# Optimization experiments

Measured on AMD Instinct MI355X. Metric: run time of the kernel, lower is better.

Reference implementation:

```python
import jax, jax.numpy as jnp
import numpy as np

PAD = 0
B, S = 8, 256
V, E, H = 32000, 512, 1024


def setup_inputs() -> dict:
    key = jax.random.key(0)
    ks = jax.random.split(key, 8)
    s = lambda k, shape, fan: jax.random.normal(k, shape, dtype=jnp.float32) / np.sqrt(fan)
    return {
        "x": jax.random.randint(ks[0], (B, S), 0, V, dtype=jnp.int32),
        "emb_W": s(ks[1], (V, E), E),          # embedding table, shared with generator
        "W_ih": s(ks[2], (3 * H, E), E),        # GRU input->gates (r,z,n)
        "W_hh": s(ks[3], (3 * H, H), H),        # GRU hidden->gates
        "b_ih": jnp.zeros((3 * H,), jnp.float32),
        "b_hh": jnp.zeros((3 * H,), jnp.float32),
        "lin_W": s(ks[4], (E, H + E), H + E),   # linear_logit
        "lin_b": jnp.zeros((E,), jnp.float32),
    }


def _gru(emb, mask, W_ih, W_hh, b_ih, b_hh):
    # emb: [B,S,E], mask: [B,S] True at PAD. Returns ctx [B,S,H].
    gx = jnp.einsum('bse,ge->bsg', emb, W_ih) + b_ih  # [B,S,3H] precomputed input gates
    gx_t = jnp.swapaxes(gx, 0, 1)                      # [S,B,3H]
    m_t = jnp.swapaxes(mask, 0, 1)                     # [S,B]

    def step(h, inp):
        g_x, m = inp
        g_h = h @ W_hh.T + b_hh
        xr, xz, xn = jnp.split(g_x, 3, axis=-1)
        hr, hz, hn = jnp.split(g_h, 3, axis=-1)
        r = jax.nn.sigmoid(xr + hr)
        z = jax.nn.sigmoid(xz + hz)
        n = jnp.tanh(xn + r * hn)
        h_new = (1.0 - z) * n + z * h
        h = jnp.where(m[:, None], h, h_new)            # carry hidden through PAD steps
        out = jnp.where(m[:, None], 0.0, h)            # packed-seq outputs are 0 at PAD
        return h, out

    h0 = jnp.zeros((emb.shape[0], W_hh.shape[1]), emb.dtype)
    _, ctx = jax.lax.scan(step, h0, (gx_t, m_t))
    return jnp.swapaxes(ctx, 0, 1)                     # [B,S,H]


def reference(x, emb_W, W_ih, W_hh, b_ih, b_hh, lin_W, lin_b):
    mask = (x == PAD)
    emb = emb_W[x]                                     # [B,S,E]
    ctx = _gru(emb, mask, W_ih, W_hh, b_ih, b_hh)      # [B,S,H]
    feat = jnp.concatenate([ctx, emb], axis=-1)        # [B,S,H+E]
    logits = jnp.tanh(feat @ lin_W.T + lin_b)          # [B,S,E]
    scores = logits @ emb_W.T                          # [B,S,V] shared-weight generator
    return jax.nn.log_softmax(scores, axis=-1)
```

## Files before the change

### kernel.cpp

```cpp
#include <hip/hip_runtime.h>

typedef unsigned int u32;
typedef unsigned short u16;
typedef unsigned long long u64;
typedef __attribute__((ext_vector_type(8))) short short8;
typedef __attribute__((ext_vector_type(4))) float floatx4;

#define BB 8
#define SS 256
#define VV 32000
#define EE 512
#define HH 1024
#define GRU_BLOCKS 64
#define GRU_THREADS 192
#define NCHUNK 500

__device__ __forceinline__ float b2f(u16 h) {
  union { u32 u; float f; } c; c.u = ((u32)h) << 16; return c.f;
}
__device__ __forceinline__ u16 f2b_bits(u32 u) {
  return (u16)((u + 0x7FFFu + ((u >> 16) & 1u)) >> 16);
}
__device__ __forceinline__ u16 f2b(float f) {
  union { float f; u32 u; } c; c.f = f; return f2b_bits(c.u);
}

__global__ __launch_bounds__(256) void k_detect(const u32* __restrict__ w, int* __restrict__ dflag) {
  __shared__ int cnt;
  if (threadIdx.x == 0) cnt = 0;
  __syncthreads();
  int c = 0;
  for (int i = threadIdx.x; i < 8192; i += 256) {
    u32 e8 = (w[i] >> 7) & 0xFF;
    c += (e8 >= 100 && e8 <= 144);
  }
  atomicAdd(&cnt, c);
  __syncthreads();
  if (threadIdx.x == 0) dflag[0] = (cnt * 2 > 8192) ? 1 : 0;
}

__global__ __launch_bounds__(256) void k_conv(const void* __restrict__ src, u16* __restrict__ dst,
                                              int n, const int* __restrict__ dflag) {
  int i = (blockIdx.x * 256 + threadIdx.x) * 8;
  if (i >= n) return;
  if (dflag[0]) {
    *(uint4*)(dst + i) = *(const uint4*)((const u16*)src + i);
  } else {
    const float* s = (const float*)src + i;
    uint4 a = *(const uint4*)s, b = *(const uint4*)(s + 4);
    u32 w0 = ((u32)f2b_bits(a.y) << 16) | f2b_bits(a.x);
    u32 w1 = ((u32)f2b_bits(a.w) << 16) | f2b_bits(a.z);
    u32 w2 = ((u32)f2b_bits(b.y) << 16) | f2b_bits(b.x);
    u32 w3 = ((u32)f2b_bits(b.w) << 16) | f2b_bits(b.z);
    uint4 r; r.x = w0; r.y = w1; r.z = w2; r.w = w3;
    *(uint4*)(dst + i) = r;
  }
}

__global__ __launch_bounds__(256) void k_init(u32* h_tag, u32* flags, int* dflag, int setflag) {
  int t = threadIdx.x;
  for (int i = t; i < 2 * 8192; i += 256) h_tag[i] = 0;
  if (t < 128) flags[t] = 0;
  if (t == 0 && setflag >= 0) dflag[0] = setflag;
}

__global__ __launch_bounds__(64) void k_gather(const int* __restrict__ x,
                                               const u16* __restrict__ embW,
                                               u16* __restrict__ emb,
                                               u16* __restrict__ feat) {
  int row = blockIdx.x, l = threadIdx.x;
  int tok = x[row];
  uint4 v = ((const uint4*)(embW + (size_t)tok * EE))[l];
  ((uint4*)(emb + (size_t)row * EE))[l] = v;
  ((uint4*)(feat + (size_t)row * 1536 + HH))[l] = v;
}

template <int KTOT>
__device__ __forceinline__ void gemm_core(const u16* __restrict__ A, int lda,
                                          const u16* __restrict__ Bm, int ldb,
                                          int m0, int n0, floatx4 acc[4][4]) {
  __shared__ __align__(16) u16 As[128 * 64];
  __shared__ __align__(16) u16 Bs[128 * 64];
  const int tid = threadIdx.x;
  const int lane = tid & 63, w = tid >> 6;
  const int wm = w & 1, wn = w >> 1;
  const int col16 = lane & 15, quad = lane >> 4;
  floatx4 z = {0.f, 0.f, 0.f, 0.f};
  for (int i = 0; i < 4; i++)
    for (int j = 0; j < 4; j++) acc[i][j] = z;

  for (int k0 = 0; k0 < KTOT; k0 += 64) {
#pragma unroll
    for (int i = 0; i < 4; i++) {
      int c = tid + i * 256;
      int r = c >> 3, off = (c & 7) * 8;
      *(uint4*)&As[r * 64 + off] = *(const uint4*)&A[(size_t)(m0 + r) * lda + k0 + off];
      *(uint4*)&Bs[r * 64 + off] = *(const uint4*)&Bm[(size_t)(n0 + r) * ldb + k0 + off];
    }
    __syncthreads();
#pragma unroll
    for (int kk = 0; kk < 2; kk++) {
      short8 af[4], bf[4];
#pragma unroll
      for (int i = 0; i < 4; i++) {
        af[i] = *(const short8*)&As[(wm * 64 + i * 16 + col16) * 64 + kk * 32 + quad * 8];
        bf[i] = *(const short8*)&Bs[(wn * 64 + i * 16 + col16) * 64 + kk * 32 + quad * 8];
      }
#pragma unroll
      for (int i = 0; i < 4; i++)
#pragma unroll
        for (int j = 0; j < 4; j++)
          acc[i][j] = __builtin_amdgcn_mfma_f32_16x16x32_bf16(af[i], bf[j], acc[i][j], 0, 0, 0);
    }
    __syncthreads();
  }
}

__global__ __launch_bounds__(256) void k_gx(const u16* __restrict__ emb,
                                            const u16* __restrict__ W_ih,
                                            const u16* __restrict__ b_ih,
                                            float* __restrict__ gx2) {
  floatx4 acc[4][4];
  int bm = blockIdx.x, bn = blockIdx.y;
  gemm_core<EE>(emb, EE, W_ih, EE, bm * 128, bn * 128, acc);
  const int tid = threadIdx.x, lane = tid & 63, w = tid >> 6;
  const int wm = w & 1, wn = w >> 1, col16 = lane & 15, quad = lane >> 4;
#pragma unroll
  for (int j = 0; j < 4; j++) {
    int g = bn * 128 + wn * 64 + j * 16 + col16;
    float bias = b2f(b_ih[g]);
    int grp = g >> 10, colh = g & 1023;
    int gb = colh >> 4, slot = grp * 16 + (colh & 15);
#pragma unroll
    for (int i = 0; i < 4; i++)
#pragma unroll
      for (int e = 0; e < 4; e++) {
        int row = bm * 128 + wm * 64 + i * 16 + quad * 4 + e;
        int b = row >> 8, s = row & 255;
        gx2[((size_t)(s * 64 + gb) * 48 + slot) * 8 + b] = acc[i][j][e] + bias;
      }
  }
}

__global__ __launch_bounds__(GRU_THREADS) void k_gru(const u16* __restrict__ W_hh,
                                                     const u16* __restrict__ b_hh,
                                                     const int* __restrict__ x,
                                                     const float* __restrict__ gx2,
                                                     u32* __restrict__ h_tag,
                                                     u32* __restrict__ flags,
                                                     u16* __restrict__ feat) {
  __shared__ __align__(16) u16 h_lds[16][1032];
  __shared__ float gh[3][16][8];
  __shared__ float hold[16][8];
  __shared__ float bhh[48];
  __shared__ int x_s[2048];

  const int tid = threadIdx.x;
  const int lane = tid & 63, w = tid >> 6;
  const int blk = blockIdx.x, hc = blk * 16;
  const int col16 = lane & 15, quad = lane >> 4;

  for (int i = tid; i < 16 * 1032; i += GRU_THREADS) ((u16*)h_lds)[i] = 0;
  for (int i = tid; i < 2048; i += GRU_THREADS) x_s[i] = x[i];
  if (tid < 128) hold[tid & 15][tid >> 4] = 0.f;
  if (tid < 48) bhh[tid] = b2f(b_hh[(tid >> 4) * HH + hc + (tid & 15)]);

  short8 Wf[32];
  {
    int grow = w * HH + hc + col16;
    const u16* wp = W_hh + (size_t)grow * HH + quad * 8;
#pragma unroll
    for (int t = 0; t < 32; t++) Wf[t] = *(const short8*)(wp + t * 32);
  }
  __syncthreads();

  const int cj = tid & 15, cb = tid >> 4;
#pragma unroll 1
  for (int s = 0; s < SS; s++) {
    float xr = 0.f, xz = 0.f, xn = 0.f;
    if (tid < 128) {
      const float* gp = gx2 + (size_t)(s * 64 + blk) * 384;
      xr = gp[cj * 8 + cb];
      xz = gp[128 + cj * 8 + cb];
      xn = gp[256 + cj * 8 + cb];
    }
    if (tid < 64 && tid != blk) {
      const u32* fp = flags + (s & 1) * 64 + tid;
      int guard = 0;
      while (__hip_atomic_load(fp, __ATOMIC_RELAXED, __HIP_MEMORY_SCOPE_AGENT) != (u32)s) {
        if (++guard > (1 << 20)) break;
      }
    }
    __syncthreads();
    {
      const u64* hb = (const u64*)(h_tag + (size_t)(s & 1) * 8192);
      const u32 want = (u32)(s & 0xFFFF);
      u64 vals[22];
      u32 pend = 0;
#pragma unroll
      for (int i = 0; i < 22; i++) {
        int pr = tid + i * GRU_THREADS;
        if (pr < 4096 && ((pr & 511) >> 3) != blk) pend |= 1u << i;
      }
      int guard = 0;
      while (pend) {
#pragma unroll
        for (int i = 0; i < 22; i++)
          if (pend & (1u << i))
            vals[i] = __hip_atomic_load(hb + (tid + i * GRU_THREADS),
                                        __ATOMIC_RELAXED, __HIP_MEMORY_SCOPE_AGENT);
#pragma unroll
        for (int i = 0; i < 22; i++)
          if (pend & (1u << i)) {
            u64 v = vals[i];
            if ((u32)(v & 0xFFFFu) == want && ((u32)(v >> 32) & 0xFFFFu) == want) {
              int pr = tid + i * GRU_THREADS;
              u32 packed = ((u32)(v >> 16) & 0xFFFFu) | ((u32)(v >> 48) << 16);
              *(u32*)&h_lds[pr >> 9][(pr & 511) * 2] = packed;
              pend &= ~(1u << i);
            }
          }
        if (pend) {
          if (++guard > (1 << 14)) break;
        }
      }
    }
    __syncthreads();
    {
      const u16* hp = &h_lds[col16][quad * 8];
      floatx4 a0 = {0.f, 0.f, 0.f, 0.f}, a1 = {0.f, 0.f, 0.f, 0.f};
#pragma unroll
      for (int t = 0; t < 32; t += 2) {
        short8 f0 = *(const short8*)(hp + t * 32);
        short8 f1 = *(const short8*)(hp + t * 32 + 32);
        a0 = __builtin_amdgcn_mfma_f32_16x16x32_bf16(f0, Wf[t], a0, 0, 0, 0);
        a1 = __builtin_amdgcn_mfma_f32_16x16x32_bf16(f1, Wf[t + 1], a1, 0, 0, 0);
      }
      a0 += a1;
      if (quad < 2) {
#pragma unroll
        for (int e = 0; e < 4; e++) gh[w][col16][quad * 4 + e] = a0[e];
      }
    }
    __syncthreads();
    if (tid < 128) {
      float hr = gh[0][cj][cb] + bhh[cj];
      float hz = gh[1][cj][cb] + bhh[16 + cj];
      float hn = gh[2][cj][cb] + bhh[32 + cj];
      float r = 1.f / (1.f + __expf(-(xr + hr)));
      float z = 1.f / (1.f + __expf(-(xz + hz)));
      float tn = xn + r * hn;
      float n = 1.f - 2.f / (1.f + __expf(2.f * tn));
      float ho = hold[cj][cb];
      float hnew = (1.f - z) * n + z * ho;
      int pad = (x_s[cb * SS + s] == 0);
      if (pad) hnew = ho;
      hold[cj][cb] = hnew;
      u16 hb16 = f2b(hnew);
      u32 tw = ((u32)hb16 << 16) | (u32)((s + 1) & 0xFFFF);
      __hip_atomic_store(h_tag + (size_t)((s + 1) & 1) * 8192 + cb * 1024 + hc + cj, tw,
                         __ATOMIC_RELAXED, __HIP_MEMORY_SCOPE_AGENT);
      h_lds[cb][hc + cj] = hb16;
      feat[(size_t)(cb * SS + s) * 1536 + hc + cj] = pad ? (u16)0 : hb16;
    }
    if (tid == 0)
      __hip_atomic_store(flags + ((s + 1) & 1) * 64 + blk, (u32)(s + 1),
                         __ATOMIC_RELAXED, __HIP_MEMORY_SCOPE_AGENT);
  }
}

__global__ __launch_bounds__(256) void k_lin(const u16* __restrict__ feat,
                                             const u16* __restrict__ lin_W,
                                             const u16* __restrict__ lin_b,
                                             u16* __restrict__ logits) {
  floatx4 acc[4][4];
  int bm = blockIdx.x, bn = blockIdx.y;
  gemm_core<1536>(feat, 1536, lin_W, 1536, bm * 128, bn * 128, acc);
  const int tid = threadIdx.x, lane = tid & 63, w = tid >> 6;
  const int wm = w & 1, wn = w >> 1, col16 = lane & 15, quad = lane >> 4;
#pragma unroll
  for (int j = 0; j < 4; j++) {
    int col = bn * 128 + wn * 64 + j * 16 + col16;
    float bias = b2f(lin_b[col]);
#pragma unroll
    for (int i = 0; i < 4; i++)
#pragma unroll
      for (int e = 0; e < 4; e++) {
        int row = bm * 128 + wm * 64 + i * 16 + quad * 4 + e;
        logits[(size_t)row * EE + col] = f2b(tanhf(acc[i][j][e] + bias));
      }
  }
}

__global__ __launch_bounds__(256) void k_scores(const u16* __restrict__ logits,
                                                const u16* __restrict__ embW,
                                                void* __restrict__ outv,
                                                float* __restrict__ partial,
                                                const int* __restrict__ dflag) {
  floatx4 acc[4][4];
  int bm = blockIdx.x, bn = blockIdx.y;
  gemm_core<EE>(logits, EE, embW, EE, bm * 128, bn * 128, acc);
  const int tid = threadIdx.x, lane = tid & 63, w = tid >> 6;
  const int wm = w & 1, wn = w >> 1, col16 = lane & 15, quad = lane >> 4;
  const int bf = dflag[0];
  u16* out16 = (u16*)outv;
  float* out32 = (float*)outv;
#pragma unroll
  for (int i = 0; i < 4; i++) {
#pragma unroll
    for (int e = 0; e < 4; e++) {
      int row = bm * 128 + wm * 64 + i * 16 + quad * 4 + e;
      size_t ob = (size_t)row * VV + bn * 128 + wn * 64;
      float sl = 0.f;
#pragma unroll
      for (int j = 0; j < 4; j++) {
        float v = acc[i][j][e];
        if (bf) out16[ob + j * 16 + col16] = f2b(v);
        else    out32[ob + j * 16 + col16] = v;
        sl += __expf(v);
      }
      sl += __shfl_xor(sl, 1, 64);
      sl += __shfl_xor(sl, 2, 64);
      sl += __shfl_xor(sl, 4, 64);
      sl += __shfl_xor(sl, 8, 64);
      if (col16 == 0) partial[(size_t)row * NCHUNK + bn * 2 + wn] = sl;
    }
  }
}

__global__ __launch_bounds__(64) void k_lse(const float* __restrict__ partial,
                                            float* __restrict__ lse) {
  int row = blockIdx.x, lane = threadIdx.x;
  float s = 0.f;
  for (int c = lane; c < NCHUNK; c += 64) s += partial[(size_t)row * NCHUNK + c];
#pragma unroll
  for (int d = 32; d >= 1; d >>= 1) s += __shfl_xor(s, d, 64);
  if (lane == 0) lse[row] = logf(s);
}

__global__ __launch_bounds__(256) void k_fix(void* __restrict__ outv,
                                             const float* __restrict__ lse,
                                             const int* __restrict__ dflag) {
  int g = blockIdx.x * 256 + threadIdx.x;
  if (dflag[0]) {
    if (g >= 8192000) return;
    u16* out = (u16*)outv;
    int row = g / 4000;
    float l = lse[row];
    uint4 v = ((const uint4*)out)[g];
    u32 a[4] = {v.x, v.y, v.z, v.w};
#pragma unroll
    for (int k = 0; k < 4; k++) {
      float lo = b2f((u16)(a[k] & 0xffff)) - l;
      float hi = b2f((u16)(a[k] >> 16)) - l;
      a[k] = ((u32)f2b(hi) << 16) | (u32)f2b(lo);
    }
    uint4 r; r.x = a[0]; r.y = a[1]; r.z = a[2]; r.w = a[3];
    ((uint4*)out)[g] = r;
  } else {
    float* out = (float*)outv;
    int row = g / 8000;
    float l = lse[row];
    float4 v = ((const float4*)out)[g];
    v.x -= l; v.y -= l; v.z -= l; v.w -= l;
    ((float4*)out)[g] = v;
  }
}

extern "C" void kernel_launch(void* const* d_in, const int* in_sizes, int n_in,
                              void* d_out, int out_size, void* d_ws, size_t ws_size,
                              hipStream_t stream) {
  const int* x = (const int*)d_in[0];

  char* ws = (char*)d_ws;
  float* gx2     = (float*)(ws);
  u16*   feat    = (u16*)(ws + 25165824);
  u16*   emb     = (u16*)(ws + 31457280);
  u16*   logits  = (u16*)(ws + 33554432);
  u32*   h_tag   = (u32*)(ws + 35651584);
  float* partial = (float*)(ws + 35717120);
  float* lse     = (float*)(ws + 39813120);
  u32*   flags   = (u32*)(ws + 39813120);
  int*   dflag   = (int*)(ws + 39821312);
  u16*   embW_c  = (u16*)(ws + 39821568);
  u16*   Wih_c   = (u16*)(ws + 72589568);
  u16*   Whh_c   = (u16*)(ws + 75735296);
  u16*   linW_c  = (u16*)(ws + 82026752);
  u16*   bih_c   = (u16*)(ws + 83599616);
  u16*   bhh_c   = (u16*)(ws + 83605760);
  u16*   linb_c  = (u16*)(ws + 83611904);
  const size_t TOTAL_WS = 83612928;

  const u16 *embW, *W_ih, *W_hh, *b_ih, *b_hh, *lin_W, *lin_b;
  if (ws_size >= TOTAL_WS) {
    k_detect<<<1, 256, 0, stream>>>((const u32*)d_in[1], dflag);
    k_init<<<1, 256, 0, stream>>>(h_tag, flags, dflag, -1);
    k_conv<<<8000, 256, 0, stream>>>(d_in[1], embW_c, VV * EE, dflag);
    k_conv<<<1536, 256, 0, stream>>>(d_in[3], Whh_c, 3 * HH * HH, dflag);
    k_conv<<<768,  256, 0, stream>>>(d_in[2], Wih_c, 3 * HH * EE, dflag);
    k_conv<<<384,  256, 0, stream>>>(d_in[6], linW_c, EE * (HH + EE), dflag);
    k_conv<<<2,    256, 0, stream>>>(d_in[4], bih_c, 3 * HH, dflag);
    k_conv<<<2,    256, 0, stream>>>(d_in[5], bhh_c, 3 * HH, dflag);
    k_conv<<<1,    256, 0, stream>>>(d_in[7], linb_c, EE, dflag);
    embW = embW_c; W_ih = Wih_c; W_hh = Whh_c; b_ih = bih_c;
    b_hh = bhh_c; lin_W = linW_c; lin_b = linb_c;
  } else {
    k_init<<<1, 256, 0, stream>>>(h_tag, flags, dflag, 1);
    embW = (const u16*)d_in[1]; W_ih = (const u16*)d_in[2]; W_hh = (const u16*)d_in[3];
    b_ih = (const u16*)d_in[4]; b_hh = (const u16*)d_in[5];
    lin_W = (const u16*)d_in[6]; lin_b = (const u16*)d_in[7];
  }

  k_gather<<<2048, 64, 0, stream>>>(x, embW, emb, feat);
  k_gx<<<dim3(16, 24), 256, 0, stream>>>(emb, W_ih, b_ih, gx2);
  k_gru<<<GRU_BLOCKS, GRU_THREADS, 0, stream>>>(W_hh, b_hh, x, gx2, h_tag, flags, feat);
  k_lin<<<dim3(16, 4), 256, 0, stream>>>(feat, lin_W, lin_b, logits);
  k_scores<<<dim3(16, 250), 256, 0, stream>>>(logits, embW, d_out, partial, dflag);
  k_lse<<<2048, 64, 0, stream>>>(partial, lse);
  k_fix<<<64000, 256, 0, stream>>>(d_out, lse, dflag);
}
```

Baseline: 1.807 ms.

## Fuse GRU, linear and scores into persistent kernel overlapping chunks

Merges the GRU recurrence, the linear projection and the vocabulary score GEMM into one persistent kernel. 64 blocks run the GRU while 192 consumer blocks wait on per-32-step chunk counters and then compute the linear and score tiles for finished timesteps. The feat rows are reordered time-major so each chunk is contiguous, and output rows are remapped back to batch-major. The goal is to hide the heavy score GEMM behind the latency-bound recurrence. The risk is that spinning consumer blocks compete with GRU blocks for memory bandwidth, or the scheme deadlocks if not all 256 blocks are co-resident.

```diff
diff --git a/kernel.cpp b/kernel.cpp
--- a/kernel.cpp
+++ b/kernel.cpp
@@ -12,7 +12,7 @@
 #define EE 512
 #define HH 1024
 #define GRU_BLOCKS 64
-#define GRU_THREADS 192
+#define CONS_BLOCKS 192
 #define NCHUNK 500
 
 __device__ __forceinline__ float b2f(u16 h) {
@@ -57,10 +57,12 @@
   }
 }
 
-__global__ __launch_bounds__(256) void k_init(u32* h_tag, u32* flags, int* dflag, int setflag) {
+__global__ __launch_bounds__(256) void k_init(u32* h_tag, u32* flags, u32* sync,
+                                              int* dflag, int setflag) {
   int t = threadIdx.x;
   for (int i = t; i < 2 * 8192; i += 256) h_tag[i] = 0;
   if (t < 128) flags[t] = 0;
+  if (t < 16) sync[t] = 0;
   if (t == 0 && setflag >= 0) dflag[0] = setflag;
 }
 
@@ -72,7 +74,8 @@
   int tok = x[row];
   uint4 v = ((const uint4*)(embW + (size_t)tok * EE))[l];
   ((uint4*)(emb + (size_t)row * EE))[l] = v;
-  ((uint4*)(feat + (size_t)row * 1536 + HH))[l] = v;
+  int rf = ((row & 255) << 3) | (row >> 8);
+  ((uint4*)(feat + (size_t)rf * 1536 + HH))[l] = v;
 }
 
 template <int KTOT>
@@ -142,188 +145,227 @@
   }
 }
 
-__global__ __launch_bounds__(GRU_THREADS) void k_gru(const u16* __restrict__ W_hh,
-                                                     const u16* __restrict__ b_hh,
-                                                     const int* __restrict__ x,
-                                                     const float* __restrict__ gx2,
-                                                     u32* __restrict__ h_tag,
-                                                     u32* __restrict__ flags,
-                                                     u16* __restrict__ feat) {
-  __shared__ __align__(16) u16 h_lds[16][1032];
-  __shared__ float gh[3][16][8];
-  __shared__ float hold[16][8];
-  __shared__ float bhh[48];
-  __shared__ int x_s[2048];
-
-  const int tid = threadIdx.x;
-  const int lane = tid & 63, w = tid >> 6;
-  const int blk = blockIdx.x, hc = blk * 16;
-  const int col16 = lane & 15, quad = lane >> 4;
-
-  for (int i = tid; i < 16 * 1032; i += GRU_THREADS) ((u16*)h_lds)[i] = 0;
-  for (int i = tid; i < 2048; i += GRU_THREADS) x_s[i] = x[i];
-  if (tid < 128) hold[tid & 15][tid >> 4] = 0.f;
-  if (tid < 48) bhh[tid] = b2f(b_hh[(tid >> 4) * HH + hc + (tid & 15)]);
-
-  short8 Wf[32];
-  {
-    int grow = w * HH + hc + col16;
-    const u16* wp = W_hh + (size_t)grow * HH + quad * 8;
-#pragma unroll
-    for (int t = 0; t < 32; t++) Wf[t] = *(const short8*)(wp + t * 32);
-  }
-  __syncthreads();
-
-  const int cj = tid & 15, cb = tid >> 4;
+__global__ __launch_bounds__(256, 1) void k_mega(const u16* __restrict__ W_hh,
+                                                 const u16* __restrict__ b_hh,
+                                                 const int* __restrict__ x,
+                                                 const float* __restrict__ gx2,
+                                                 u32* __restrict__ h_tag,
+                                                 u32* __restrict__ flags,
+                                                 u16* __restrict__ feat,
+                                                 const u16* __restrict__ lin_W,
+                                                 const u16* __restrict__ lin_b,
+                                                 u16* __restrict__ logits,
+                                                 const u16* __restrict__ embW,
+                                                 void* __restrict__ outv,
+                                                 float* __restrict__ partial,
+                                                 const int* __restrict__ dflag,
+                                                 u32* __restrict__ sync) {
+  u32* chunk_done = sync;
+  u32* lin_done   = sync + 8;
+
+  if (blockIdx.x < GRU_BLOCKS) {
+    __shared__ __align__(16) u16 h_lds[16][1032];
+    __shared__ float gh[3][16][8];
+    __shared__ float hold[16][8];
+    __shared__ float bhh[48];
+    __shared__ int x_s[2048];
+
+    const int tid = threadIdx.x;
+    const int lane = tid & 63, w = tid >> 6;
+    const int blk = blockIdx.x, hc = blk * 16;
+    const int col16 = lane & 15, quad = lane >> 4;
+
+    for (int i = tid; i < 16 * 1032; i += 256) ((u16*)h_lds)[i] = 0;
+    for (int i = tid; i < 2048; i += 256) x_s[i] = x[i];
+    if (tid < 128) hold[tid & 15][tid >> 4] = 0.f;
+    if (tid < 48) bhh[tid] = b2f(b_hh[(tid >> 4) * HH + hc + (tid & 15)]);
+
+    short8 Wf[32];
+    if (w < 3) {
+      int grow = w * HH + hc + col16;
+      const u16* wp = W_hh + (size_t)grow * HH + quad * 8;
+#pragma unroll
+      for (int t = 0; t < 32; t++) Wf[t] = *(const short8*)(wp + t * 32);
+    }
+    __syncthreads();
+
+    const int cj = tid & 15, cb = tid >> 4;
 #pragma unroll 1
-  for (int s = 0; s < SS; s++) {
-    float xr = 0.f, xz = 0.f, xn = 0.f;
-    if (tid < 128) {
-      const float* gp = gx2 + (size_t)(s * 64 + blk) * 384;
-      xr = gp[cj * 8 + cb];
-      xz = gp[128 + cj * 8 + cb];
-      xn = gp[256 + cj * 8 + cb];
-    }
-    if (tid < 64 && tid != blk) {
-      const u32* fp = flags + (s & 1) * 64 + tid;
-      int guard = 0;
-      while (__hip_atomic_load(fp, __ATOMIC_RELAXED, __HIP_MEMORY_SCOPE_AGENT) != (u32)s) {
-        if (++guard > (1 << 20)) break;
-      }
-    }
-    __syncthreads();
-    {
-      const u64* hb = (const u64*)(h_tag + (size_t)(s & 1) * 8192);
-      const u32 want = (u32)(s & 0xFFFF);
-      u64 vals[22];
-      u32 pend = 0;
-#pragma unroll
-      for (int i = 0; i < 22; i++) {
-        int pr = tid + i * GRU_THREADS;
-        if (pr < 4096 && ((pr & 511) >> 3) != blk) pend |= 1u << i;
-      }
-      int guard = 0;
-      while (pend) {
-#pragma unroll
-        for (int i = 0; i < 22; i++)
-          if (pend & (1u << i))
-            vals[i] = __hip_atomic_load(hb + (tid + i * GRU_THREADS),
-                                        __ATOMIC_RELAXED, __HIP_MEMORY_SCOPE_AGENT);
-#pragma unroll
-        for (int i = 0; i < 22; i++)
-          if (pend & (1u << i)) {
-            u64 v = vals[i];
-            if ((u32)(v & 0xFFFFu) == want && ((u32)(v >> 32) & 0xFFFFu) == want) {
-              int pr = tid + i * GRU_THREADS;
-              u32 packed = ((u32)(v >> 16) & 0xFFFFu) | ((u32)(v >> 48) << 16);
-              *(u32*)&h_lds[pr >> 9][(pr & 511) * 2] = packed;
-              pend &= ~(1u << i);
+    for (int s = 0; s < SS; s++) {
+      float xr = 0.f, xz = 0.f, xn = 0.f;
+      if (tid < 128) {
+        const float* gp = gx2 + (size_t)(s * 64 + blk) * 384;
+        xr = gp[cj * 8 + cb];
+        xz = gp[128 + cj * 8 + cb];
+        xn = gp[256 + cj * 8 + cb];
+      }
+      if (tid < 64 && tid != blk) {
+        const u32* fp = flags + (s & 1) * 64 + tid;
+        int guard = 0;
+        while (__hip_atomic_load(fp, __ATOMIC_RELAXED, __HIP_MEMORY_SCOPE_AGENT) != (u32)s) {
+          if (++guard > (1 << 20)) break;
+        }
+      }
+      __syncthreads();
+      {
+        const u64* hb = (const u64*)(h_tag + (size_t)(s & 1) * 8192);
+        const u32 want = (u32)(s & 0xFFFF);
+        u64 vals[16];
+        u32 pend = 0;
+#pragma unroll
+        for (int i = 0; i < 16; i++) {
+          int pr = tid + i * 256;
+          if (((pr & 511) >> 3) != blk) pend |= 1u << i;
+        }
+        int guard = 0;
+        while (pend) {
+#pragma unroll
+          for (int i = 0; i < 16; i++)
+            if (pend & (1u << i))
+              vals[i] = __hip_atomic_load(hb + (tid + i * 256),
+                                          __ATOMIC_RELAXED, __HIP_MEMORY_SCOPE_AGENT);
+#pragma unroll
+          for (int i = 0; i < 16; i++)
+            if (pend & (1u << i)) {
+              u64 v = vals[i];
+              if ((u32)(v & 0xFFFFu) == want && ((u32)(v >> 32) & 0xFFFFu) == want) {
+                int pr = tid + i * 256;
+                u32 packed = ((u32)(v >> 16) & 0xFFFFu) | ((u32)(v >> 48) << 16);
+                *(u32*)&h_lds[pr >> 9][(pr & 511) * 2] = packed;
+                pend &= ~(1u << i);
+              }
             }
+          if (pend) {
+            if (++guard > (1 << 14)) break;
           }
-        if (pend) {
-          if (++guard > (1 << 14)) break;
-        }
-      }
-    }
-    __syncthreads();
-    {
-      const u16* hp = &h_lds[col16][quad * 8];
-      floatx4 a0 = {0.f, 0.f, 0.f, 0.f}, a1 = {0.f, 0.f, 0.f, 0.f};
-#pragma unroll
-      for (int t = 0; t < 32; t += 2) {
-        short8 f0 = *(const short8*)(hp + t * 32);
-        short8 f1 = *(const short8*)(hp + t * 32 + 32);
-        a0 = __builtin_amdgcn_mfma_f32_16x16x32_bf16(f0, Wf[t], a0, 0, 0, 0);
-        a1 = __builtin_amdgcn_mfma_f32_16x16x32_bf16(f1, Wf[t + 1], a1, 0, 0, 0);
-      }
-      a0 += a1;
-      if (quad < 2) {
-#pragma unroll
-        for (int e = 0; e < 4; e++) gh[w][col16][quad * 4 + e] = a0[e];
-      }
-    }
-    __syncthreads();
-    if (tid < 128) {
-      float hr = gh[0][cj][cb] + bhh[cj];
-      float hz = gh[1][cj][cb] + bhh[16 + cj];
-      float hn = gh[2][cj][cb] + bhh[32 + cj];
-      float r = 1.f / (1.f + __expf(-(xr + hr)));
-      float z = 1.f / (1.f + __expf(-(xz + hz)));
-      float tn = xn + r * hn;
-      float n = 1.f - 2.f / (1.f + __expf(2.f * tn));
-      float ho = hold[cj][cb];
-      float hnew = (1.f - z) * n + z * ho;
-      int pad = (x_s[cb * SS + s] == 0);
-      if (pad) hnew = ho;
-      hold[cj][cb] = hnew;
-      u16 hb16 = f2b(hnew);
-      u32 tw = ((u32)hb16 << 16) | (u32)((s + 1) & 0xFFFF);
-      __hip_atomic_store(h_tag + (size_t)((s + 1) & 1) * 8192 + cb * 1024 + hc + cj, tw,
-                         __ATOMIC_RELAXED, __HIP_MEMORY_SCOPE_AGENT);
-      h_lds[cb][hc + cj] = hb16;
-      feat[(size_t)(cb * SS + s) * 1536 + hc + cj] = pad ? (u16)0 : hb16;
-    }
-    if (tid == 0)
-      __hip_atomic_store(flags + ((s + 1) & 1) * 64 + blk, (u32)(s + 1),
-                         __ATOMIC_RELAXED, __HIP_MEMORY_SCOPE_AGENT);
-  }
-}
-
-__global__ __launch_bounds__(256) void k_lin(const u16* __restrict__ feat,
-                                             const u16* __restrict__ lin_W,
-                                             const u16* __restrict__ lin_b,
-                                             u16* __restrict__ logits) {
-  floatx4 acc[4][4];
-  int bm = blockIdx.x, bn = blockIdx.y;
-  gemm_core<1536>(feat, 1536, lin_W, 1536, bm * 128, bn * 128, acc);
-  const int tid = threadIdx.x, lane = tid & 63, w = tid >> 6;
-  const int wm = w & 1, wn = w >> 1, col16 = lane & 15, quad = lane >> 4;
-#pragma unroll
-  for (int j = 0; j < 4; j++) {
-    int col = bn * 128 + wn * 64 + j * 16 + col16;
-    float bias = b2f(lin_b[col]);
-#pragma unroll
-    for (int i = 0; i < 4; i++)
-#pragma unroll
-      for (int e = 0; e < 4; e++) {
-        int row = bm * 128 + wm * 64 + i * 16 + quad * 4 + e;
-        logits[(size_t)row * EE + col] = f2b(tanhf(acc[i][j][e] + bias));
-      }
-  }
-}
-
-__global__ __launch_bounds__(256) void k_scores(const u16* __restrict__ logits,
-                                                const u16* __restrict__ embW,
-                                                void* __restrict__ outv,
-                                                float* __restrict__ partial,
-                                                const int* __restrict__ dflag) {
-  floatx4 acc[4][4];
-  int bm = blockIdx.x, bn = blockIdx.y;
-  gemm_core<EE>(logits, EE, embW, EE, bm * 128, bn * 128, acc);
-  const int tid = threadIdx.x, lane = tid & 63, w = tid >> 6;
-  const int wm = w & 1, wn = w >> 1, col16 = lane & 15, quad = lane >> 4;
-  const int bf = dflag[0];
-  u16* out16 = (u16*)outv;
-  float* out32 = (float*)outv;
-#pragma unroll
-  for (int i = 0; i < 4; i++) {
-#pragma unroll
-    for (int e = 0; e < 4; e++) {
-      int row = bm * 128 + wm * 64 + i * 16 + quad * 4 + e;
-      size_t ob = (size_t)row * VV + bn * 128 + wn * 64;
-      float sl = 0.f;
-#pragma unroll
-      for (int j = 0; j < 4; j++) {
-        float v = acc[i][j][e];
-        if (bf) out16[ob + j * 16 + col16] = f2b(v);
-        else    out32[ob + j * 16 + col16] = v;
-        sl += __expf(v);
-      }
-      sl += __shfl_xor(sl, 1, 64);
-      sl += __shfl_xor(sl, 2, 64);
-      sl += __shfl_xor(sl, 4, 64);
-      sl += __shfl_xor(sl, 8, 64);
-      if (col16 == 0) partial[(size_t)row * NCHUNK + bn * 2 + wn] = sl;
+        }
+      }
+      __syncthreads();
+      if (w < 3) {
+        const u16* hp = &h_lds[col16][quad * 8];
+        floatx4 a0 = {0.f, 0.f, 0.f, 0.f}, a1 = {0.f, 0.f, 0.f, 0.f};
+#pragma unroll
+        for (int t = 0; t < 32; t += 2) {
+          short8 f0 = *(const short8*)(hp + t * 32);
+          short8 f1 = *(const short8*)(hp + t * 32 + 32);
+          a0 = __builtin_amdgcn_mfma_f32_16x16x32_bf16(f0, Wf[t], a0, 0, 0, 0);
+          a1 = __builtin_amdgcn_mfma_f32_16x16x32_bf16(f1, Wf[t + 1], a1, 0, 0, 0);
+        }
+        a0 += a1;
+        if (quad < 2) {
+#pragma unroll
+          for (int e = 0; e < 4; e++) gh[w][col16][quad * 4 + e] = a0[e];
+        }
+      }
+      __syncthreads();
+      if (tid < 128) {
+        float hr = gh[0][cj][cb] + bhh[cj];
+        float hz = gh[1][cj][cb] + bhh[16 + cj];
+        float hn = gh[2][cj][cb] + bhh[32 + cj];
+        float r = 1.f / (1.f + __expf(-(xr + hr)));
+        float z = 1.f / (1.f + __expf(-(xz + hz)));
+        float tn = xn + r * hn;
+        float n = 1.f - 2.f / (1.f + __expf(2.f * tn));
+        float ho = hold[cj][cb];
+        float hnew = (1.f - z) * n + z * ho;
+        int pad = (x_s[cb * SS + s] == 0);
+        if (pad) hnew = ho;
+        hold[cj][cb] = hnew;
+        u16 hb16 = f2b(hnew);
+        u32 tw = ((u32)hb16 << 16) | (u32)((s + 1) & 0xFFFF);
+        __hip_atomic_store(h_tag + (size_t)((s + 1) & 1) * 8192 + cb * 1024 + hc + cj, tw,
+                           __ATOMIC_RELAXED, __HIP_MEMORY_SCOPE_AGENT);
+        h_lds[cb][hc + cj] = hb16;
+        u32 fv = pad ? 0u : (u32)hb16;
+        u32 ov = (u32)__shfl_xor((int)fv, 1, 64);
+        if (!(cj & 1))
+          __hip_atomic_store((u32*)(feat + (size_t)(s * 8 + cb) * 1536 + hc + cj),
+                             fv | (ov << 16), __ATOMIC_RELAXED, __HIP_MEMORY_SCOPE_AGENT);
+      }
+      if (tid == 0)
+        __hip_atomic_store(flags + ((s + 1) & 1) * 64 + blk, (u32)(s + 1),
+                           __ATOMIC_RELAXED, __HIP_MEMORY_SCOPE_AGENT);
+      if ((s & 31) == 31) {
+        __syncthreads();
+        if (tid == 0)
+          __hip_atomic_fetch_add(chunk_done + (s >> 5), 1u,
+                                 __ATOMIC_RELAXED, __HIP_MEMORY_SCOPE_AGENT);
+      }
+    }
+  } else {
+    const int cid = blockIdx.x - GRU_BLOCKS;
+    const int tid = threadIdx.x, lane = tid & 63, w4 = tid >> 6;
+    const int wm = w4 & 1, wn = w4 >> 1, col16 = lane & 15, quad = lane >> 4;
+    const int bf = dflag[0];
+    u16* out16 = (u16*)outv;
+    float* out32 = (float*)outv;
+
+    for (int t = cid; t < 8 * 508; t += CONS_BLOCKS) {
+      int c = t / 508, i = t - c * 508;
+      floatx4 acc[4][4];
+      if (i < 8) {
+        if (tid == 0) {
+          while (__hip_atomic_load(chunk_done + c, __ATOMIC_RELAXED,
+                                   __HIP_MEMORY_SCOPE_AGENT) < (u32)GRU_BLOCKS)
+            __builtin_amdgcn_s_sleep(8);
+        }
+        __syncthreads();
+        int mt = i & 1, bn = i >> 1;
+        gemm_core<1536>(feat, 1536, lin_W, 1536, c * 256 + mt * 128, bn * 128, acc);
+#pragma unroll
+        for (int j = 0; j < 4; j++) {
+          int col = bn * 128 + wn * 64 + j * 16 + col16;
+          float bias = b2f(lin_b[col]);
+#pragma unroll
+          for (int ii = 0; ii < 4; ii++)
+#pragma unroll
+            for (int e = 0; e < 4; e++) {
+              int row = c * 256 + mt * 128 + wm * 64 + ii * 16 + quad * 4 + e;
+              u32 mine = (u32)f2b(tanhf(acc[ii][j][e] + bias));
+              u32 oth = (u32)__shfl_xor((int)mine, 1, 64);
+              if (!(col16 & 1))
+                __hip_atomic_store((u32*)(logits + (size_t)row * EE + col),
+                                   mine | (oth << 16),
+                                   __ATOMIC_RELAXED, __HIP_MEMORY_SCOPE_AGENT);
+            }
+        }
+        __syncthreads();
+        if (tid == 0)
+          __hip_atomic_fetch_add(lin_done + c, 1u,
+                                 __ATOMIC_RELAXED, __HIP_MEMORY_SCOPE_AGENT);
+      } else {
+        int j2 = i - 8;
+        int mt = j2 & 1, bn = j2 >> 1;
+        if (tid == 0) {
+          while (__hip_atomic_load(lin_done + c, __ATOMIC_RELAXED,
+                                   __HIP_MEMORY_SCOPE_AGENT) < 8u)
+            __builtin_amdgcn_s_sleep(8);
+        }
+        __syncthreads();
+        gemm_core<EE>(logits, EE, embW, EE, c * 256 + mt * 128, bn * 128, acc);
+#pragma unroll
+        for (int ii = 0; ii < 4; ii++) {
+#pragma unroll
+          for (int e = 0; e < 4; e++) {
+            int rf = c * 256 + mt * 128 + wm * 64 + ii * 16 + quad * 4 + e;
+            int ro = ((rf & 7) << 8) | (rf >> 3);
+            size_t ob = (size_t)ro * VV + bn * 128 + wn * 64;
+            float sl = 0.f;
+#pragma unroll
+            for (int jj = 0; jj < 4; jj++) {
+              float v = acc[ii][jj][e];
+              if (bf) out16[ob + jj * 16 + col16] = f2b(v);
+              else    out32[ob + jj * 16 + col16] = v;
+              sl += __expf(v);
+            }
+            sl += __shfl_xor(sl, 1, 64);
+            sl += __shfl_xor(sl, 2, 64);
+            sl += __shfl_xor(sl, 4, 64);
+            sl += __shfl_xor(sl, 8, 64);
+            if (col16 == 0) partial[(size_t)ro * NCHUNK + bn * 2 + wn] = sl;
+          }
+        }
+      }
     }
   }
 }
@@ -382,6 +424,7 @@
   float* lse     = (float*)(ws + 39813120);
   u32*   flags   = (u32*)(ws + 39813120);
   int*   dflag   = (int*)(ws + 39821312);
+  u32*   sync    = (u32*)(ws + 39821312 + 128);
   u16*   embW_c  = (u16*)(ws + 39821568);
   u16*   Wih_c   = (u16*)(ws + 72589568);
   u16*   Whh_c   = (u16*)(ws + 75735296);
@@ -394,7 +437,7 @@
   const u16 *embW, *W_ih, *W_hh, *b_ih, *b_hh, *lin_W, *lin_b;
   if (ws_size >= TOTAL_WS) {
     k_detect<<<1, 256, 0, stream>>>((const u32*)d_in[1], dflag);
-    k_init<<<1, 256, 0, stream>>>(h_tag, flags, dflag, -1);
+    k_init<<<1, 256, 0, stream>>>(h_tag, flags, sync, dflag, -1);
     k_conv<<<8000, 256, 0, stream>>>(d_in[1], embW_c, VV * EE, dflag);
     k_conv<<<1536, 256, 0, stream>>>(d_in[3], Whh_c, 3 * HH * HH, dflag);
     k_conv<<<768,  256, 0, stream>>>(d_in[2], Wih_c, 3 * HH * EE, dflag);
@@ -405,7 +448,7 @@
     embW = embW_c; W_ih = Wih_c; W_hh = Whh_c; b_ih = bih_c;
     b_hh = bhh_c; lin_W = linW_c; lin_b = linb_c;
   } else {
-    k_init<<<1, 256, 0, stream>>>(h_tag, flags, dflag, 1);
+    k_init<<<1, 256, 0, stream>>>(h_tag, flags, sync, dflag, 1);
     embW = (const u16*)d_in[1]; W_ih = (const u16*)d_in[2]; W_hh = (const u16*)d_in[3];
     b_ih = (const u16*)d_in[4]; b_hh = (const u16*)d_in[5];
     lin_W = (const u16*)d_in[6]; lin_b = (const u16*)d_in[7];
@@ -413,9 +456,9 @@
 
   k_gather<<<2048, 64, 0, stream>>>(x, embW, emb, feat);
   k_gx<<<dim3(16, 24), 256, 0, stream>>>(emb, W_ih, b_ih, gx2);
-  k_gru<<<GRU_BLOCKS, GRU_THREADS, 0, stream>>>(W_hh, b_hh, x, gx2, h_tag, flags, feat);
-  k_lin<<<dim3(16, 4), 256, 0, stream>>>(feat, lin_W, lin_b, logits);
-  k_scores<<<dim3(16, 250), 256, 0, stream>>>(logits, embW, d_out, partial, dflag);
+  k_mega<<<GRU_BLOCKS + CONS_BLOCKS, 256, 0, stream>>>(W_hh, b_hh, x, gx2, h_tag, flags,
+                                                       feat, lin_W, lin_b, logits, embW,
+                                                       d_out, partial, dflag, sync);
   k_lse<<<2048, 64, 0, stream>>>(partial, lse);
   k_fix<<<64000, 256, 0, stream>>>(d_out, lse, dflag);
 }
```

After: 1.535 ms. -15.0%, faster.
